# Performance work log

Hardware: AMD Instinct MI355X
Metric: run time of the kernel (lower is better)

Reference implementation:

```python
import jax, jax.numpy as jnp
import numpy as np

EPS = 1e-9
TEMP = 1.0
TOP_K = 2


def setup_inputs() -> dict:
    key = jax.random.key(0)
    k1, k2, k3, k4 = jax.random.split(key, 4)
    B, T, D, DC, E = 8, 4096, 1024, 512, 64
    din = D + DC
    inputs = jax.random.normal(k1, (B, T, D), dtype=jnp.float32)
    cond = jax.random.normal(k2, (B, T, DC), dtype=jnp.float32)
    # CondRouterMLP params (bias=False): Linear(din -> 2*din), GELU, Linear(2*din -> E)
    W1 = jax.random.normal(k3, (2 * din, din), dtype=jnp.float32) / np.sqrt(din).astype(np.float32)
    W2 = jax.random.normal(k4, (E, 2 * din), dtype=jnp.float32) / np.sqrt(2 * din).astype(np.float32)
    return {"inputs": inputs, "cond": cond, "W1": W1, "W2": W2}


def reference(inputs, cond, W1, W2):
    B, T, D = inputs.shape
    # concat hidden states with condition, flatten tokens
    x = jnp.concatenate([inputs, cond], axis=-1).reshape(-1, D + cond.shape[-1])  # [N, din]
    h = jax.nn.gelu(x @ W1.T, approximate=False)          # [N, 2*din] (torch nn.GELU = exact erf)
    logits = h @ W2.T                                     # [N, E]
    logits = (logits - logits.max(axis=-1, keepdims=True)) / TEMP
    probs = jax.nn.softmax(logits, axis=-1) + EPS
    probs = jnp.clip(probs, EPS, 1.0 - EPS)               # [N, E]
    # eval-mode top-k selection
    top_v, top_i = jax.lax.top_k(probs, TOP_K)            # [N, k]
    N, E = probs.shape
    rows = jnp.arange(N)[:, None]
    router_mask = jnp.zeros_like(probs).at[rows, top_i].set(1.0)
    router_probs = jnp.zeros_like(probs).at[rows, top_i].set(top_v)
    router_probs = router_probs / router_probs.sum(axis=-1, keepdims=True)  # normalize=True
    return (
        router_mask.reshape(B, T, E),
        top_i.reshape(B, T, TOP_K),
        router_probs.reshape(B, T, E),
        probs.reshape(B, T, E),
    )
```

## Files before the change

kernel.cpp:

```cpp
#include <hip/hip_runtime.h>
#include <cmath>

#define N_TOK 32768
#define D0    1024
#define DCC   512
#define DIN   1536
#define JD    3072
#define NE    64
#define BM    128
#define BJ    128
#define KC    32
#define NJC   (JD/BJ)
#define NKS   (DIN/KC)
#define NTH   512
#define HS    36
#define EPSV  1e-9f

typedef _Float16 half8 __attribute__((ext_vector_type(8)));
typedef float    f32x4 __attribute__((ext_vector_type(4)));

#define SZ_BUF 16384
#define OFF_A  0
#define OFF_B  32768
#define OFF_H  65536
#define LDS_TOTAL (OFF_H + 8*4608)
#define OFF_LRED OFF_H
#define OFF_EPI  OFF_A

#define W1T_G (192*3072)
#define W2T_G (384*64)

__device__ __forceinline__ f32x4 mfma16(half8 a, half8 b, f32x4 c) {
    return __builtin_amdgcn_mfma_f32_16x16x32_f16(a, b, c, 0, 0, 0);
}

__device__ __forceinline__ void split8(const float4 v0, const float4 v1, half8& hh, half8& hl) {
    float f[8] = {v0.x, v0.y, v0.z, v0.w, v1.x, v1.y, v1.z, v1.w};
    #pragma unroll
    for (int i = 0; i < 8; ++i) {
        _Float16 h = (_Float16)f[i];
        hh[i] = h;
        hl[i] = (_Float16)(f[i] - (float)h);
    }
}

__device__ __forceinline__ void gload16(const void* g, void* l) {
    __builtin_amdgcn_global_load_lds(
        (const __attribute__((address_space(1))) unsigned int*)g,
        (__attribute__((address_space(3))) unsigned int*)l, 16, 0, 0);
}

__global__ void presplit_w1t(const float* __restrict__ W1,
                             _Float16* __restrict__ hi, _Float16* __restrict__ lo) {
    int g = blockIdx.x * blockDim.x + threadIdx.x;
    if (g >= W1T_G) return;
    const int j  = g % JD;
    const int ko = g / JD;
    const float* src = W1 + (size_t)j * DIN + ko * 8;
    float4 v0 = *(const float4*)src;
    float4 v1 = *(const float4*)(src + 4);
    half8 h, l;
    split8(v0, v1, h, l);
    *(half8*)(hi + (size_t)g * 8) = h;
    *(half8*)(lo + (size_t)g * 8) = l;
}

__global__ void presplit_w2t(const float* __restrict__ W2,
                             _Float16* __restrict__ hi, _Float16* __restrict__ lo) {
    int g = blockIdx.x * blockDim.x + threadIdx.x;
    if (g >= W2T_G) return;
    const int e  = g & 63;
    const int jo = g >> 6;
    const float* src = W2 + (size_t)e * JD + jo * 8;
    float4 v0 = *(const float4*)src;
    float4 v1 = *(const float4*)(src + 4);
    half8 h, l;
    split8(v0, v1, h, l);
    *(half8*)(hi + (size_t)g * 8) = h;
    *(half8*)(lo + (size_t)g * 8) = l;
}

__global__ __launch_bounds__(NTH, 1)
void router_v7(const float* __restrict__ inp, const float* __restrict__ cnd,
               const _Float16* __restrict__ W1h, const _Float16* __restrict__ W1l,
               const _Float16* __restrict__ W2h, const _Float16* __restrict__ W2l,
               float* __restrict__ out_mask, float* __restrict__ out_topi,
               float* __restrict__ out_rp, float* __restrict__ out_probs)
{
    __shared__ __align__(16) char smem[LDS_TOTAL];

    const int tid  = threadIdx.x;
    const int lane = tid & 63;
    const int w    = tid >> 6;
    const int tg   = w >> 1;
    const int jg   = w & 1;
    const int l15  = lane & 15;
    const int lg   = lane >> 4;
    const int t0   = blockIdx.x * BM;

    _Float16* const sHh = (_Float16*)(smem + OFF_H + w * 4608);
    _Float16* const sHl = sHh + 1152;

    const int srow  = tid >> 2;
    const int sslot = tid & 3;
    const int bplane = w >> 2;
    const int bslot  = w & 3;

    int aoffB[2], boffB[4];
    #pragma unroll
    for (int tf = 0; tf < 2; ++tf) aoffB[tf] = (lg*128 + tg*32 + tf*16 + l15) * 16;
    #pragma unroll
    for (int jf = 0; jf < 4; ++jf) boffB[jf] = (lg*128 + jg*64 + jf*16 + l15) * 16;

    const f32x4 vzero = {0.f, 0.f, 0.f, 0.f};
    f32x4 lacc[2][4];
    #pragma unroll
    for (int tf = 0; tf < 2; ++tf)
        #pragma unroll
        for (int ef = 0; ef < 4; ++ef) lacc[tf][ef] = vzero;

    const float* const xA = inp + (size_t)(t0 + srow) * D0;
    const float* const xC = cnd + (size_t)(t0 + srow) * DCC;
    const _Float16* const W1p = bplane ? W1l : W1h;

    for (int jc = 0; jc < NJC; ++jc) {
        f32x4 acc1[2][4];
        #pragma unroll
        for (int tf = 0; tf < 2; ++tf)
            #pragma unroll
            for (int jf = 0; jf < 4; ++jf) acc1[tf][jf] = vzero;

        {
            const _Float16* wsrc = W1p + ((size_t)(0*4 + bslot) * JD + jc*BJ) * 8;
            char* bb = smem + OFF_B + (bplane*512 + bslot*128) * 16;
            gload16(wsrc + (size_t)lane * 8, bb);
            gload16(wsrc + (size_t)(64 + lane) * 8, bb + 64*16);
            float4 ra0 = *(const float4*)(xA + sslot*8);
            float4 ra1 = *(const float4*)(xA + sslot*8 + 4);
            half8 hh, hl;
            split8(ra0, ra1, hh, hl);
            char* ab = smem + OFF_A;
            *(half8*)(ab + (sslot*128 + srow)*16) = hh;
            *(half8*)(ab + 8192 + (sslot*128 + srow)*16) = hl;
        }
        __syncthreads();

        int cur = 0;
        for (int ks = 0; ks < NKS; ++ks) {
            const bool more = (ks + 1 < NKS);
            const int nbuf = cur ^ 1;
            float4 ra0, ra1;
            if (more) {
                const int k = (ks + 1) * KC + sslot*8;
                const float* sA = (k < D0) ? (xA + k) : (xC + k - D0);
                ra0 = *(const float4*)sA;
                ra1 = *(const float4*)(sA + 4);
                const _Float16* wsrc = W1p + ((size_t)((ks+1)*4 + bslot) * JD + jc*BJ) * 8;
                char* bb = smem + OFF_B + nbuf*SZ_BUF + (bplane*512 + bslot*128) * 16;
                gload16(wsrc + (size_t)lane * 8, bb);
                gload16(wsrc + (size_t)(64 + lane) * 8, bb + 64*16);
            }
            const char* ab = smem + OFF_A + cur*SZ_BUF;
            const char* bb = smem + OFF_B + cur*SZ_BUF;
            half8 ah[2], al[2], bh[4], bl[4];
            #pragma unroll
            for (int tf = 0; tf < 2; ++tf) {
                ah[tf] = *(const half8*)(ab + aoffB[tf]);
                al[tf] = *(const half8*)(ab + 8192 + aoffB[tf]);
            }
            #pragma unroll
            for (int jf = 0; jf < 4; ++jf) {
                bh[jf] = *(const half8*)(bb + boffB[jf]);
                bl[jf] = *(const half8*)(bb + 8192 + boffB[jf]);
            }
            #pragma unroll
            for (int tf = 0; tf < 2; ++tf)
                #pragma unroll
                for (int jf = 0; jf < 4; ++jf) {
                    acc1[tf][jf] = mfma16(ah[tf], bh[jf], acc1[tf][jf]);
                    acc1[tf][jf] = mfma16(ah[tf], bl[jf], acc1[tf][jf]);
                    acc1[tf][jf] = mfma16(al[tf], bh[jf], acc1[tf][jf]);
                }
            if (more) {
                half8 hh, hl;
                split8(ra0, ra1, hh, hl);
                char* nab = smem + OFF_A + nbuf*SZ_BUF;
                *(half8*)(nab + (sslot*128 + srow)*16) = hh;
                *(half8*)(nab + 8192 + (sslot*128 + srow)*16) = hl;
            }
            __syncthreads();
            cur = nbuf;
        }

        #pragma unroll
        for (int h2 = 0; h2 < 2; ++h2) {
            #pragma unroll
            for (int c = 0; c < 2; ++c) {
                const int jf = h2*2 + c;
                #pragma unroll
                for (int tf = 0; tf < 2; ++tf)
                    #pragma unroll
                    for (int r = 0; r < 4; ++r) {
                        const float v = acc1[tf][jf][r];
                        const float g = 0.5f * v * (1.0f + erff(v * 0.70710678118654752f));
                        const _Float16 gh = (_Float16)g;
                        const _Float16 gl = (_Float16)(g - (float)gh);
                        const int o = (tf*16 + lg*4 + r) * HS + c*16 + l15;
                        sHh[o] = gh; sHl[o] = gl;
                    }
            }
            const int joct0 = jc*16 + jg*8 + h2*4;
            half8 a2h[2], a2l[2];
            #pragma unroll
            for (int tf = 0; tf < 2; ++tf) {
                const int o = (tf*16 + l15) * HS + lg*8;
                a2h[tf] = *(const half8*)(sHh + o);
                a2l[tf] = *(const half8*)(sHl + o);
            }
            #pragma unroll
            for (int ef = 0; ef < 4; ++ef) {
                const size_t wg = ((size_t)(joct0 + lg) * 64 + ef*16 + l15) * 8;
                half8 b2h = *(const half8*)(W2h + wg);
                half8 b2l = *(const half8*)(W2l + wg);
                #pragma unroll
                for (int tf = 0; tf < 2; ++tf) {
                    lacc[tf][ef] = mfma16(a2h[tf], b2h, lacc[tf][ef]);
                    lacc[tf][ef] = mfma16(a2h[tf], b2l, lacc[tf][ef]);
                    lacc[tf][ef] = mfma16(a2l[tf], b2h, lacc[tf][ef]);
                }
            }
        }
    }

    __syncthreads();
    float* const Lred = (float*)(smem + OFF_LRED);
    if (jg == 1) {
        #pragma unroll
        for (int tf = 0; tf < 2; ++tf)
            #pragma unroll
            for (int ef = 0; ef < 4; ++ef)
                #pragma unroll
                for (int r = 0; r < 4; ++r)
                    Lred[(tg*32 + tf*16 + lg*4 + r) * 68 + ef*16 + l15] = lacc[tf][ef][r];
    }
    __syncthreads();
    if (jg == 0) {
        #pragma unroll
        for (int tf = 0; tf < 2; ++tf)
            #pragma unroll
            for (int ef = 0; ef < 4; ++ef)
                #pragma unroll
                for (int r = 0; r < 4; ++r) {
                    const int o = (tg*32 + tf*16 + lg*4 + r) * 68 + ef*16 + l15;
                    Lred[o] += lacc[tf][ef][r];
                }
    }
    __syncthreads();

    float* const mA   = (float*)(smem + OFF_EPI);
    float* const invA = mA + BM;
    int*   const i1A  = (int*)(invA + BM);
    int*   const i2A  = i1A + BM;
    float* const rp1A = (float*)(i2A + BM);
    float* const rp2A = rp1A + BM;

    if (tid < BM) {
        const float* row = Lred + tid * 68;
        float m = -3.402823466e38f;
        for (int e = 0; e < NE; ++e) m = fmaxf(m, row[e]);
        float s = 0.f, v1 = -3.402823466e38f, v2 = -3.402823466e38f;
        int i1 = 0, i2 = 0;
        for (int e = 0; e < NE; ++e) {
            const float v = row[e];
            s += expf(v - m);
            if (v > v1)      { v2 = v1; i2 = i1; v1 = v; i1 = e; }
            else if (v > v2) { v2 = v; i2 = e; }
        }
        const float inv = 1.f / s;
        const float p1 = fminf(expf(v1 - m) * inv + EPSV, 1.f - EPSV);
        const float p2 = fminf(expf(v2 - m) * inv + EPSV, 1.f - EPSV);
        mA[tid] = m; invA[tid] = inv; i1A[tid] = i1; i2A[tid] = i2;
        const float den = p1 + p2;
        rp1A[tid] = p1 / den; rp2A[tid] = p2 / den;
    }
    __syncthreads();

    for (int idx = tid; idx < BM * NE; idx += NTH) {
        const int r = idx >> 6, e = idx & 63;
        const size_t o = (size_t)(t0 + r) * NE + e;
        const float p = fminf(expf(Lred[r * 68 + e] - mA[r]) * invA[r] + EPSV, 1.f - EPSV);
        const int b1 = (e == i1A[r]), b2 = (e == i2A[r]);
        out_probs[o] = p;
        out_mask[o]  = (b1 | b2) ? 1.f : 0.f;
        out_rp[o]    = b1 ? rp1A[r] : (b2 ? rp2A[r] : 0.f);
    }
    if (tid < BM * 2) {
        const int r = tid >> 1, q = tid & 1;
        out_topi[(size_t)(t0 + r) * 2 + q] = (float)(q ? i2A[r] : i1A[r]);
    }
}

extern "C" void kernel_launch(void* const* d_in, const int* in_sizes, int n_in,
                              void* d_out, int out_size, void* d_ws, size_t ws_size,
                              hipStream_t stream) {
    const float* inp = (const float*)d_in[0];
    const float* cnd = (const float*)d_in[1];
    const float* W1  = (const float*)d_in[2];
    const float* W2  = (const float*)d_in[3];

    float* out = (float*)d_out;
    const size_t NT = (size_t)N_TOK;
    float* out_mask  = out;
    float* out_topi  = out + NT * NE;
    float* out_rp    = out + NT * NE + NT * 2;
    float* out_probs = out + NT * NE + NT * 2 + NT * NE;

    _Float16* W1h = (_Float16*)d_ws;
    _Float16* W1l = W1h + (size_t)W1T_G * 8;
    _Float16* W2h = W1l + (size_t)W1T_G * 8;
    _Float16* W2l = W2h + (size_t)W2T_G * 8;

    hipLaunchKernelGGL(presplit_w1t, dim3((W1T_G + 255) / 256), dim3(256), 0, stream, W1, W1h, W1l);
    hipLaunchKernelGGL(presplit_w2t, dim3((W2T_G + 255) / 256), dim3(256), 0, stream, W2, W2h, W2l);
    hipLaunchKernelGGL(router_v7, dim3(N_TOK / BM), dim3(NTH), 0, stream,
                       inp, cnd, W1h, W1l, W2h, W2l,
                       out_mask, out_topi, out_rp, out_probs);
}
```

Baseline: 1.281 ms.

## Double K-tile depth to 64, swizzle A tile in LDS, reorganize smem

Raises the K step of the first GEMM from 32 to 64, so each double-buffered stage holds twice as much A and W1 data. This halves the number of barriers and loop iterations across the 1536-deep reduction. The A tile is now stored with an XOR swizzle on the row index to reduce LDS bank conflicts on the MFMA fragment reads. LDS grows to 128KB, with the GELU scratch area aliased onto the A buffers, which requires an extra barrier per j-chunk. More registers are also held for the prefetched activations.

```diff
diff --git a/kernel.cpp b/kernel.cpp
--- a/kernel.cpp
+++ b/kernel.cpp
@@ -9,9 +9,9 @@
 #define NE    64
 #define BM    128
 #define BJ    128
-#define KC    32
+#define BK    64
 #define NJC   (JD/BJ)
-#define NKS   (DIN/KC)
+#define NIT   (DIN/BK)
 #define NTH   512
 #define HS    36
 #define EPSV  1e-9f
@@ -19,13 +19,13 @@
 typedef _Float16 half8 __attribute__((ext_vector_type(8)));
 typedef float    f32x4 __attribute__((ext_vector_type(4)));
 
-#define SZ_BUF 16384
+#define SZ_BUF 32768
 #define OFF_A  0
-#define OFF_B  32768
-#define OFF_H  65536
-#define LDS_TOTAL (OFF_H + 8*4608)
-#define OFF_LRED OFF_H
-#define OFF_EPI  OFF_A
+#define OFF_B  65536
+#define LDS_TOTAL 131072
+#define OFF_H    0
+#define OFF_LRED 65536
+#define OFF_EPI  (65536 + 34816)
 
 #define W1T_G (192*3072)
 #define W2T_G (384*64)
@@ -81,7 +81,7 @@
 }
 
 __global__ __launch_bounds__(NTH, 1)
-void router_v7(const float* __restrict__ inp, const float* __restrict__ cnd,
+void router_v8(const float* __restrict__ inp, const float* __restrict__ cnd,
                const _Float16* __restrict__ W1h, const _Float16* __restrict__ W1l,
                const _Float16* __restrict__ W2h, const _Float16* __restrict__ W2l,
                float* __restrict__ out_mask, float* __restrict__ out_topi,
@@ -101,16 +101,11 @@
     _Float16* const sHh = (_Float16*)(smem + OFF_H + w * 4608);
     _Float16* const sHl = sHh + 1152;
 
-    const int srow  = tid >> 2;
-    const int sslot = tid & 3;
-    const int bplane = w >> 2;
-    const int bslot  = w & 3;
-
-    int aoffB[2], boffB[4];
-    #pragma unroll
-    for (int tf = 0; tf < 2; ++tf) aoffB[tf] = (lg*128 + tg*32 + tf*16 + l15) * 16;
-    #pragma unroll
-    for (int jf = 0; jf < 4; ++jf) boffB[jf] = (lg*128 + jg*64 + jf*16 + l15) * 16;
+    const int arow  = tid >> 2;
+    const int aslot = tid & 3;
+
+    const int bplane = w & 1;
+    const int bk0    = (w >> 1) * 2;
 
     const f32x4 vzero = {0.f, 0.f, 0.f, 0.f};
     f32x4 lacc[2][4];
@@ -119,9 +114,9 @@
         #pragma unroll
         for (int ef = 0; ef < 4; ++ef) lacc[tf][ef] = vzero;
 
-    const float* const xA = inp + (size_t)(t0 + srow) * D0;
-    const float* const xC = cnd + (size_t)(t0 + srow) * DCC;
-    const _Float16* const W1p = bplane ? W1l : W1h;
+    const float* const xA = inp + (size_t)(t0 + arow) * D0;
+    const float* const xC = cnd + (size_t)(t0 + arow) * DCC;
+    const _Float16* const Wbp = bplane ? W1l : W1h;
 
     for (int jc = 0; jc < NJC; ++jc) {
         f32x4 acc1[2][4];
@@ -131,72 +126,98 @@
             for (int jf = 0; jf < 4; ++jf) acc1[tf][jf] = vzero;
 
         {
-            const _Float16* wsrc = W1p + ((size_t)(0*4 + bslot) * JD + jc*BJ) * 8;
-            char* bb = smem + OFF_B + (bplane*512 + bslot*128) * 16;
-            gload16(wsrc + (size_t)lane * 8, bb);
-            gload16(wsrc + (size_t)(64 + lane) * 8, bb + 64*16);
-            float4 ra0 = *(const float4*)(xA + sslot*8);
-            float4 ra1 = *(const float4*)(xA + sslot*8 + 4);
-            half8 hh, hl;
-            split8(ra0, ra1, hh, hl);
-            char* ab = smem + OFF_A;
-            *(half8*)(ab + (sslot*128 + srow)*16) = hh;
-            *(half8*)(ab + 8192 + (sslot*128 + srow)*16) = hl;
+            #pragma unroll
+            for (int q = 0; q < 2; ++q) {
+                const int ko = bk0 + q;
+                const _Float16* src = Wbp + ((size_t)ko * JD + jc * BJ) * 8;
+                char* dst = smem + OFF_B + ((bplane * 8 + ko) * 128) * 16;
+                gload16(src + (size_t)lane * 8, dst);
+                gload16(src + (size_t)(64 + lane) * 8, dst + 1024);
+            }
+            #pragma unroll
+            for (int q2 = 0; q2 < 2; ++q2) {
+                const int koct = aslot * 2 + q2;
+                const int k = koct * 8;
+                const float* sx = (k < D0) ? (xA + k) : (xC + k - D0);
+                float4 v0 = *(const float4*)sx;
+                float4 v1 = *(const float4*)(sx + 4);
+                half8 hh, hl;
+                split8(v0, v1, hh, hl);
+                const int g = koct * 128 + (arow ^ (koct & 7));
+                *(half8*)(smem + OFF_A + g * 16) = hh;
+                *(half8*)(smem + OFF_A + (1024 + g) * 16) = hl;
+            }
         }
         __syncthreads();
 
-        int cur = 0;
-        for (int ks = 0; ks < NKS; ++ks) {
-            const bool more = (ks + 1 < NKS);
-            const int nbuf = cur ^ 1;
-            float4 ra0, ra1;
+        for (int it = 0; it < NIT; ++it) {
+            const int cur = it & 1, nxt = cur ^ 1;
+            const bool more = (it + 1 < NIT);
+            float4 xv[4];
             if (more) {
-                const int k = (ks + 1) * KC + sslot*8;
-                const float* sA = (k < D0) ? (xA + k) : (xC + k - D0);
-                ra0 = *(const float4*)sA;
-                ra1 = *(const float4*)(sA + 4);
-                const _Float16* wsrc = W1p + ((size_t)((ks+1)*4 + bslot) * JD + jc*BJ) * 8;
-                char* bb = smem + OFF_B + nbuf*SZ_BUF + (bplane*512 + bslot*128) * 16;
-                gload16(wsrc + (size_t)lane * 8, bb);
-                gload16(wsrc + (size_t)(64 + lane) * 8, bb + 64*16);
-            }
-            const char* ab = smem + OFF_A + cur*SZ_BUF;
-            const char* bb = smem + OFF_B + cur*SZ_BUF;
-            half8 ah[2], al[2], bh[4], bl[4];
-            #pragma unroll
-            for (int tf = 0; tf < 2; ++tf) {
-                ah[tf] = *(const half8*)(ab + aoffB[tf]);
-                al[tf] = *(const half8*)(ab + 8192 + aoffB[tf]);
-            }
-            #pragma unroll
-            for (int jf = 0; jf < 4; ++jf) {
-                bh[jf] = *(const half8*)(bb + boffB[jf]);
-                bl[jf] = *(const half8*)(bb + 8192 + boffB[jf]);
-            }
-            #pragma unroll
-            for (int tf = 0; tf < 2; ++tf)
+                #pragma unroll
+                for (int q = 0; q < 2; ++q) {
+                    const int ko = (it + 1) * 8 + bk0 + q;
+                    const _Float16* src = Wbp + ((size_t)ko * JD + jc * BJ) * 8;
+                    char* dst = smem + OFF_B + nxt * SZ_BUF + ((bplane * 8 + bk0 + q) * 128) * 16;
+                    gload16(src + (size_t)lane * 8, dst);
+                    gload16(src + (size_t)(64 + lane) * 8, dst + 1024);
+                }
+                #pragma unroll
+                for (int q2 = 0; q2 < 2; ++q2) {
+                    const int k = (it + 1) * BK + (aslot * 2 + q2) * 8;
+                    const float* sx = (k < D0) ? (xA + k) : (xC + k - D0);
+                    xv[q2 * 2]     = *(const float4*)sx;
+                    xv[q2 * 2 + 1] = *(const float4*)(sx + 4);
+                }
+            }
+            const char* ab = smem + OFF_A + cur * SZ_BUF;
+            const char* bb = smem + OFF_B + cur * SZ_BUF;
+            #pragma unroll
+            for (int ks2 = 0; ks2 < 2; ++ks2) {
+                const int c = ks2 * 4 + lg;
+                half8 ah[2], al[2], bh[4], bl[4];
+                #pragma unroll
+                for (int tf = 0; tf < 2; ++tf) {
+                    const int g = c * 128 + ((tg * 32 + tf * 16 + l15) ^ c);
+                    ah[tf] = *(const half8*)(ab + g * 16);
+                    al[tf] = *(const half8*)(ab + (1024 + g) * 16);
+                }
                 #pragma unroll
                 for (int jf = 0; jf < 4; ++jf) {
-                    acc1[tf][jf] = mfma16(ah[tf], bh[jf], acc1[tf][jf]);
-                    acc1[tf][jf] = mfma16(ah[tf], bl[jf], acc1[tf][jf]);
-                    acc1[tf][jf] = mfma16(al[tf], bh[jf], acc1[tf][jf]);
-                }
+                    const int g = c * 128 + (jg * 64 + jf * 16 + l15);
+                    bh[jf] = *(const half8*)(bb + g * 16);
+                    bl[jf] = *(const half8*)(bb + (1024 + g) * 16);
+                }
+                #pragma unroll
+                for (int tf = 0; tf < 2; ++tf)
+                    #pragma unroll
+                    for (int jf = 0; jf < 4; ++jf) {
+                        acc1[tf][jf] = mfma16(ah[tf], bh[jf], acc1[tf][jf]);
+                        acc1[tf][jf] = mfma16(ah[tf], bl[jf], acc1[tf][jf]);
+                        acc1[tf][jf] = mfma16(al[tf], bh[jf], acc1[tf][jf]);
+                    }
+            }
             if (more) {
-                half8 hh, hl;
-                split8(ra0, ra1, hh, hl);
-                char* nab = smem + OFF_A + nbuf*SZ_BUF;
-                *(half8*)(nab + (sslot*128 + srow)*16) = hh;
-                *(half8*)(nab + 8192 + (sslot*128 + srow)*16) = hl;
+                char* nab = smem + OFF_A + nxt * SZ_BUF;
+                #pragma unroll
+                for (int q2 = 0; q2 < 2; ++q2) {
+                    const int koct = aslot * 2 + q2;
+                    half8 hh, hl;
+                    split8(xv[q2 * 2], xv[q2 * 2 + 1], hh, hl);
+                    const int g = koct * 128 + (arow ^ (koct & 7));
+                    *(half8*)(nab + g * 16) = hh;
+                    *(half8*)(nab + (1024 + g) * 16) = hl;
+                }
             }
             __syncthreads();
-            cur = nbuf;
         }
 
         #pragma unroll
         for (int h2 = 0; h2 < 2; ++h2) {
             #pragma unroll
             for (int c = 0; c < 2; ++c) {
-                const int jf = h2*2 + c;
+                const int jf = h2 * 2 + c;
                 #pragma unroll
                 for (int tf = 0; tf < 2; ++tf)
                     #pragma unroll
@@ -205,21 +226,21 @@
                         const float g = 0.5f * v * (1.0f + erff(v * 0.70710678118654752f));
                         const _Float16 gh = (_Float16)g;
                         const _Float16 gl = (_Float16)(g - (float)gh);
-                        const int o = (tf*16 + lg*4 + r) * HS + c*16 + l15;
+                        const int o = (tf * 16 + lg * 4 + r) * HS + c * 16 + l15;
                         sHh[o] = gh; sHl[o] = gl;
                     }
             }
-            const int joct0 = jc*16 + jg*8 + h2*4;
+            const int joct0 = jc * 16 + jg * 8 + h2 * 4;
             half8 a2h[2], a2l[2];
             #pragma unroll
             for (int tf = 0; tf < 2; ++tf) {
-                const int o = (tf*16 + l15) * HS + lg*8;
+                const int o = (tf * 16 + l15) * HS + lg * 8;
                 a2h[tf] = *(const half8*)(sHh + o);
                 a2l[tf] = *(const half8*)(sHl + o);
             }
             #pragma unroll
             for (int ef = 0; ef < 4; ++ef) {
-                const size_t wg = ((size_t)(joct0 + lg) * 64 + ef*16 + l15) * 8;
+                const size_t wg = ((size_t)(joct0 + lg) * 64 + ef * 16 + l15) * 8;
                 half8 b2h = *(const half8*)(W2h + wg);
                 half8 b2l = *(const half8*)(W2l + wg);
                 #pragma unroll
@@ -230,9 +251,9 @@
                 }
             }
         }
-    }
-
-    __syncthreads();
+        __syncthreads();
+    }
+
     float* const Lred = (float*)(smem + OFF_LRED);
     if (jg == 1) {
         #pragma unroll
@@ -322,7 +343,7 @@
 
     hipLaunchKernelGGL(presplit_w1t, dim3((W1T_G + 255) / 256), dim3(256), 0, stream, W1, W1h, W1l);
     hipLaunchKernelGGL(presplit_w2t, dim3((W2T_G + 255) / 256), dim3(256), 0, stream, W2, W2h, W2l);
-    hipLaunchKernelGGL(router_v7, dim3(N_TOK / BM), dim3(NTH), 0, stream,
+    hipLaunchKernelGGL(router_v8, dim3(N_TOK / BM), dim3(NTH), 0, stream,
                        inp, cnd, W1h, W1l, W2h, W2l,
                        out_mask, out_topi, out_rp, out_probs);
 }
```

After: 1.117 ms. -12.8%, faster.

## Widen hidden-dim tile to 256 and split second GEMM by expert across warps

Applied to the files above, without the earlier changes.

Doubles the hidden-dimension chunk per iteration (BJ 128→256) with a 2x4 warp layout where each warp computes a 64x64 tile, halving the number of times the activation tile is re-read and split per block. The second GEMM is reorganised so each warp owns 16 experts and reads the GELU tiles of its row-group peers through shared memory, removing the final cross-warp logits reduction. This adds extra barriers per chunk and doubles the LDS footprint and accumulator registers, which may raise register pressure.

```diff
diff --git a/kernel.cpp b/kernel.cpp
--- a/kernel.cpp
+++ b/kernel.cpp
@@ -8,10 +8,10 @@
 #define JD    3072
 #define NE    64
 #define BM    128
-#define BJ    128
-#define KC    32
+#define BJ    256
+#define BK    32
 #define NJC   (JD/BJ)
-#define NKS   (DIN/KC)
+#define NIT   (DIN/BK)
 #define NTH   512
 #define HS    36
 #define EPSV  1e-9f
@@ -19,13 +19,14 @@
 typedef _Float16 half8 __attribute__((ext_vector_type(8)));
 typedef float    f32x4 __attribute__((ext_vector_type(4)));
 
-#define SZ_BUF 16384
-#define OFF_A  0
-#define OFF_B  32768
-#define OFF_H  65536
-#define LDS_TOTAL (OFF_H + 8*4608)
-#define OFF_LRED OFF_H
-#define OFF_EPI  OFF_A
+#define SZ_A  16384
+#define SZ_B  32768
+#define OFF_A 0
+#define OFF_B 32768
+#define LDS_TOTAL 98304
+#define OFF_H    0
+#define OFF_LRED 0
+#define OFF_EPI  36864
 
 #define W1T_G (192*3072)
 #define W2T_G (384*64)
@@ -81,7 +82,7 @@
 }
 
 __global__ __launch_bounds__(NTH, 1)
-void router_v7(const float* __restrict__ inp, const float* __restrict__ cnd,
+void router_v9(const float* __restrict__ inp, const float* __restrict__ cnd,
                const _Float16* __restrict__ W1h, const _Float16* __restrict__ W1l,
                const _Float16* __restrict__ W2h, const _Float16* __restrict__ W2l,
                float* __restrict__ out_mask, float* __restrict__ out_topi,
@@ -92,89 +93,90 @@
     const int tid  = threadIdx.x;
     const int lane = tid & 63;
     const int w    = tid >> 6;
-    const int tg   = w >> 1;
-    const int jg   = w & 1;
+    const int tg   = w >> 2;
+    const int jg   = w & 3;
     const int l15  = lane & 15;
     const int lg   = lane >> 4;
     const int t0   = blockIdx.x * BM;
 
-    _Float16* const sHh = (_Float16*)(smem + OFF_H + w * 4608);
-    _Float16* const sHl = sHh + 1152;
-
-    const int srow  = tid >> 2;
-    const int sslot = tid & 3;
+    const int akoct = w >> 1;
+    const int arow  = (w & 1) * 64 + lane;
     const int bplane = w >> 2;
-    const int bslot  = w & 3;
-
-    int aoffB[2], boffB[4];
+    const int bkoct  = w & 3;
+
+    int aoff[4], boff[4];
     #pragma unroll
-    for (int tf = 0; tf < 2; ++tf) aoffB[tf] = (lg*128 + tg*32 + tf*16 + l15) * 16;
+    for (int tf = 0; tf < 4; ++tf) aoff[tf] = (lg*128 + tg*64 + tf*16 + l15) * 16;
     #pragma unroll
-    for (int jf = 0; jf < 4; ++jf) boffB[jf] = (lg*128 + jg*64 + jf*16 + l15) * 16;
+    for (int jf = 0; jf < 4; ++jf) boff[jf] = (lg*256 + jg*64 + jf*16 + l15) * 16;
 
     const f32x4 vzero = {0.f, 0.f, 0.f, 0.f};
-    f32x4 lacc[2][4];
-    #pragma unroll
-    for (int tf = 0; tf < 2; ++tf)
+    f32x4 lacc[4] = {vzero, vzero, vzero, vzero};
+
+    const float* const xrowA = inp + (size_t)(t0 + arow) * D0;
+    const float* const xrowC = cnd + (size_t)(t0 + arow) * DCC;
+    const _Float16* const Wbp = bplane ? W1l : W1h;
+
+    _Float16* const myHh = (_Float16*)(smem + OFF_H + w * 9216);
+    _Float16* const myHl = myHh + 2304;
+
+    for (int jc = 0; jc < NJC; ++jc) {
+        f32x4 acc1[4][4];
         #pragma unroll
-        for (int ef = 0; ef < 4; ++ef) lacc[tf][ef] = vzero;
-
-    const float* const xA = inp + (size_t)(t0 + srow) * D0;
-    const float* const xC = cnd + (size_t)(t0 + srow) * DCC;
-    const _Float16* const W1p = bplane ? W1l : W1h;
-
-    for (int jc = 0; jc < NJC; ++jc) {
-        f32x4 acc1[2][4];
-        #pragma unroll
-        for (int tf = 0; tf < 2; ++tf)
+        for (int tf = 0; tf < 4; ++tf)
             #pragma unroll
             for (int jf = 0; jf < 4; ++jf) acc1[tf][jf] = vzero;
 
         {
-            const _Float16* wsrc = W1p + ((size_t)(0*4 + bslot) * JD + jc*BJ) * 8;
-            char* bb = smem + OFF_B + (bplane*512 + bslot*128) * 16;
-            gload16(wsrc + (size_t)lane * 8, bb);
-            gload16(wsrc + (size_t)(64 + lane) * 8, bb + 64*16);
-            float4 ra0 = *(const float4*)(xA + sslot*8);
-            float4 ra1 = *(const float4*)(xA + sslot*8 + 4);
+            #pragma unroll
+            for (int q = 0; q < 4; ++q) {
+                const _Float16* src = Wbp + ((size_t)bkoct * JD + jc*BJ + q*64 + lane) * 8;
+                char* dst = smem + OFF_B + bplane*16384 + bkoct*4096 + q*1024;
+                gload16(src, dst);
+            }
+            const float* sx = xrowA + akoct * 8;
+            float4 v0 = *(const float4*)sx;
+            float4 v1 = *(const float4*)(sx + 4);
             half8 hh, hl;
-            split8(ra0, ra1, hh, hl);
-            char* ab = smem + OFF_A;
-            *(half8*)(ab + (sslot*128 + srow)*16) = hh;
-            *(half8*)(ab + 8192 + (sslot*128 + srow)*16) = hl;
+            split8(v0, v1, hh, hl);
+            const int g = (akoct*128 + arow) * 16;
+            *(half8*)(smem + OFF_A + g) = hh;
+            *(half8*)(smem + OFF_A + 8192 + g) = hl;
         }
         __syncthreads();
 
-        int cur = 0;
-        for (int ks = 0; ks < NKS; ++ks) {
-            const bool more = (ks + 1 < NKS);
-            const int nbuf = cur ^ 1;
-            float4 ra0, ra1;
+        for (int it = 0; it < NIT; ++it) {
+            const int cur = it & 1, nxt = cur ^ 1;
+            const bool more = (it + 1 < NIT);
+            float4 xv0, xv1;
             if (more) {
-                const int k = (ks + 1) * KC + sslot*8;
-                const float* sA = (k < D0) ? (xA + k) : (xC + k - D0);
-                ra0 = *(const float4*)sA;
-                ra1 = *(const float4*)(sA + 4);
-                const _Float16* wsrc = W1p + ((size_t)((ks+1)*4 + bslot) * JD + jc*BJ) * 8;
-                char* bb = smem + OFF_B + nbuf*SZ_BUF + (bplane*512 + bslot*128) * 16;
-                gload16(wsrc + (size_t)lane * 8, bb);
-                gload16(wsrc + (size_t)(64 + lane) * 8, bb + 64*16);
-            }
-            const char* ab = smem + OFF_A + cur*SZ_BUF;
-            const char* bb = smem + OFF_B + cur*SZ_BUF;
-            half8 ah[2], al[2], bh[4], bl[4];
-            #pragma unroll
-            for (int tf = 0; tf < 2; ++tf) {
-                ah[tf] = *(const half8*)(ab + aoffB[tf]);
-                al[tf] = *(const half8*)(ab + 8192 + aoffB[tf]);
+                const int ko = (it + 1) * 4 + bkoct;
+                #pragma unroll
+                for (int q = 0; q < 4; ++q) {
+                    const _Float16* src = Wbp + ((size_t)ko * JD + jc*BJ + q*64 + lane) * 8;
+                    char* dst = smem + OFF_B + nxt*SZ_B + bplane*16384 + bkoct*4096 + q*1024;
+                    gload16(src, dst);
+                }
+                const int k = (it + 1) * BK + akoct * 8;
+                const float* sx = (k < D0) ? (xrowA + k) : (xrowC + k - D0);
+                xv0 = *(const float4*)sx;
+                xv1 = *(const float4*)(sx + 4);
+            }
+            const char* ab = smem + OFF_A + cur*SZ_A;
+            const char* bb = smem + OFF_B + cur*SZ_B;
+            half8 ah[4], al[4], bh[4], bl[4];
+            #pragma unroll
+            for (int tf = 0; tf < 4; ++tf) {
+                ah[tf] = *(const half8*)(ab + aoff[tf]);
+                al[tf] = *(const half8*)(ab + 8192 + aoff[tf]);
             }
             #pragma unroll
             for (int jf = 0; jf < 4; ++jf) {
-                bh[jf] = *(const half8*)(bb + boffB[jf]);
-                bl[jf] = *(const half8*)(bb + 8192 + boffB[jf]);
-            }
-            #pragma unroll
-            for (int tf = 0; tf < 2; ++tf)
+                bh[jf] = *(const half8*)(bb + boff[jf]);
+                bl[jf] = *(const half8*)(bb + 16384 + boff[jf]);
+            }
+            #pragma unroll
+            for (int tf = 0; tf < 4; ++tf)
                 #pragma unroll
                 for (int jf = 0; jf < 4; ++jf) {
                     acc1[tf][jf] = mfma16(ah[tf], bh[jf], acc1[tf][jf]);
@@ -183,78 +185,60 @@
                 }
             if (more) {
                 half8 hh, hl;
-                split8(ra0, ra1, hh, hl);
-                char* nab = smem + OFF_A + nbuf*SZ_BUF;
-                *(half8*)(nab + (sslot*128 + srow)*16) = hh;
-                *(half8*)(nab + 8192 + (sslot*128 + srow)*16) = hl;
+                split8(xv0, xv1, hh, hl);
+                const int g = (akoct*128 + arow) * 16;
+                *(half8*)(smem + OFF_A + nxt*SZ_A + g) = hh;
+                *(half8*)(smem + OFF_A + nxt*SZ_A + 8192 + g) = hl;
             }
             __syncthreads();
-            cur = nbuf;
         }
 
         #pragma unroll
-        for (int h2 = 0; h2 < 2; ++h2) {
+        for (int r = 0; r < 2; ++r) {
             #pragma unroll
             for (int c = 0; c < 2; ++c) {
-                const int jf = h2*2 + c;
+                const int jf = 2*r + c;
                 #pragma unroll
-                for (int tf = 0; tf < 2; ++tf)
+                for (int tf = 0; tf < 4; ++tf)
                     #pragma unroll
-                    for (int r = 0; r < 4; ++r) {
-                        const float v = acc1[tf][jf][r];
-                        const float g = 0.5f * v * (1.0f + erff(v * 0.70710678118654752f));
-                        const _Float16 gh = (_Float16)g;
-                        const _Float16 gl = (_Float16)(g - (float)gh);
-                        const int o = (tf*16 + lg*4 + r) * HS + c*16 + l15;
-                        sHh[o] = gh; sHl[o] = gl;
+                    for (int rr = 0; rr < 4; ++rr) {
+                        const float v = acc1[tf][jf][rr];
+                        const float gv = 0.5f * v * (1.0f + erff(v * 0.70710678118654752f));
+                        const _Float16 gh = (_Float16)gv;
+                        const _Float16 gl = (_Float16)(gv - (float)gh);
+                        const int o = (tf*16 + lg*4 + rr) * HS + c*16 + l15;
+                        myHh[o] = gh; myHl[o] = gl;
                     }
             }
-            const int joct0 = jc*16 + jg*8 + h2*4;
-            half8 a2h[2], a2l[2];
-            #pragma unroll
-            for (int tf = 0; tf < 2; ++tf) {
-                const int o = (tf*16 + l15) * HS + lg*8;
-                a2h[tf] = *(const half8*)(sHh + o);
-                a2l[tf] = *(const half8*)(sHl + o);
-            }
-            #pragma unroll
-            for (int ef = 0; ef < 4; ++ef) {
-                const size_t wg = ((size_t)(joct0 + lg) * 64 + ef*16 + l15) * 8;
+            __syncthreads();
+            #pragma unroll
+            for (int s = 0; s < 4; ++s) {
+                const _Float16* sh = (const _Float16*)(smem + OFF_H + (tg*4 + s) * 9216);
+                const _Float16* sl = sh + 2304;
+                const int jo = jc*32 + s*8 + r*4 + lg;
+                const size_t wg = ((size_t)jo * 64 + jg*16 + l15) * 8;
                 half8 b2h = *(const half8*)(W2h + wg);
                 half8 b2l = *(const half8*)(W2l + wg);
                 #pragma unroll
-                for (int tf = 0; tf < 2; ++tf) {
-                    lacc[tf][ef] = mfma16(a2h[tf], b2h, lacc[tf][ef]);
-                    lacc[tf][ef] = mfma16(a2h[tf], b2l, lacc[tf][ef]);
-                    lacc[tf][ef] = mfma16(a2l[tf], b2h, lacc[tf][ef]);
+                for (int tf = 0; tf < 4; ++tf) {
+                    const int o = (tf*16 + l15) * HS + lg*8;
+                    half8 a2h = *(const half8*)(sh + o);
+                    half8 a2l = *(const half8*)(sl + o);
+                    lacc[tf] = mfma16(a2h, b2h, lacc[tf]);
+                    lacc[tf] = mfma16(a2h, b2l, lacc[tf]);
+                    lacc[tf] = mfma16(a2l, b2h, lacc[tf]);
                 }
             }
+            __syncthreads();
         }
     }
 
-    __syncthreads();
     float* const Lred = (float*)(smem + OFF_LRED);
-    if (jg == 1) {
+    #pragma unroll
+    for (int tf = 0; tf < 4; ++tf)
         #pragma unroll
-        for (int tf = 0; tf < 2; ++tf)
-            #pragma unroll
-            for (int ef = 0; ef < 4; ++ef)
-                #pragma unroll
-                for (int r = 0; r < 4; ++r)
-                    Lred[(tg*32 + tf*16 + lg*4 + r) * 68 + ef*16 + l15] = lacc[tf][ef][r];
-    }
-    __syncthreads();
-    if (jg == 0) {
-        #pragma unroll
-        for (int tf = 0; tf < 2; ++tf)
-            #pragma unroll
-            for (int ef = 0; ef < 4; ++ef)
-                #pragma unroll
-                for (int r = 0; r < 4; ++r) {
-                    const int o = (tg*32 + tf*16 + lg*4 + r) * 68 + ef*16 + l15;
-                    Lred[o] += lacc[tf][ef][r];
-                }
-    }
+        for (int rr = 0; rr < 4; ++rr)
+            Lred[(tg*64 + tf*16 + lg*4 + rr) * 68 + jg*16 + l15] = lacc[tf][rr];
     __syncthreads();
 
     float* const mA   = (float*)(smem + OFF_EPI);
@@ -322,7 +306,7 @@
 
     hipLaunchKernelGGL(presplit_w1t, dim3((W1T_G + 255) / 256), dim3(256), 0, stream, W1, W1h, W1l);
     hipLaunchKernelGGL(presplit_w2t, dim3((W2T_G + 255) / 256), dim3(256), 0, stream, W2, W2h, W2l);
-    hipLaunchKernelGGL(router_v7, dim3(N_TOK / BM), dim3(NTH), 0, stream,
+    hipLaunchKernelGGL(router_v9, dim3(N_TOK / BM), dim3(NTH), 0, stream,
                        inp, cnd, W1h, W1l, W2h, W2l,
                        out_mask, out_topi, out_rp, out_probs);
 }
```

After: 1.098 ms. 1.17x faster.
